# Performance work log

Hardware: AMD Instinct MI355X
Metric: run time of the kernel (lower is better)

The kernel has to match this reference:

```python
import jax, jax.numpy as jnp
import numpy as np


def setup_inputs() -> dict:
    key = jax.random.key(0)
    k1, k2 = jax.random.split(key)
    decoder_hidden = jax.random.normal(k1, (16, 1024, 1024), dtype=jnp.float32)
    encoder_outputs = jax.random.normal(k2, (16, 2048, 1024), dtype=jnp.float32)
    return {"decoder_hidden": decoder_hidden, "encoder_outputs": encoder_outputs}


def reference(decoder_hidden, encoder_outputs):
    # scores: [B, Q, K] = decoder_hidden @ encoder_outputs^T (no scaling, per source)
    scores = jnp.einsum('bqd,bkd->bqk', decoder_hidden, encoder_outputs)
    attn = jax.nn.softmax(scores, axis=-1)
    # context: [B, Q, D]
    context = jnp.einsum('bqk,bkd->bqd', attn, encoder_outputs)
    return (context, attn)
```

## Files before the change

### kernel.cpp

```cpp
#include <hip/hip_runtime.h>


typedef __attribute__((ext_vector_type(8))) short s8v;
typedef __attribute__((ext_vector_type(4))) float f32x4;
typedef __attribute__((ext_vector_type(8))) unsigned short us8;
typedef __attribute__((ext_vector_type(4))) unsigned short us4;

__device__ inline unsigned short f2bf(float f) {
    unsigned u = __builtin_bit_cast(unsigned, f);
    u += 0x7FFFu + ((u >> 16) & 1u);
    return (unsigned short)(u >> 16);
}
__device__ inline float bf2f(unsigned short h) {
    return __builtin_bit_cast(float, (unsigned)h << 16);
}

__device__ __forceinline__ s8v lds_read128(unsigned addr) {
    s8v d;
    asm volatile("ds_read_b128 %0, %1" : "=v"(d) : "v"(addr));
    return d;
}

__global__ __launch_bounds__(256)
void split_convert(const float* __restrict__ x, unsigned short* __restrict__ hi,
                   unsigned short* __restrict__ lo, int n4)
{
    int i = blockIdx.x * 256 + threadIdx.x;
    const int stride = gridDim.x * 256;
    for (; i < n4; i += stride) {
        const float4 v = reinterpret_cast<const float4*>(x)[i];
        us4 h, l;
        h.x = f2bf(v.x); l.x = f2bf(v.x - bf2f(h.x));
        h.y = f2bf(v.y); l.y = f2bf(v.y - bf2f(h.y));
        h.z = f2bf(v.z); l.z = f2bf(v.z - bf2f(h.z));
        h.w = f2bf(v.w); l.w = f2bf(v.w - bf2f(h.w));
        reinterpret_cast<us4*>(hi)[i] = h;
        reinterpret_cast<us4*>(lo)[i] = l;
    }
}

__global__ __launch_bounds__(256)
void split_convert_enc(const float* __restrict__ enc,
                       unsigned short* __restrict__ encH,
                       unsigned short* __restrict__ encL,
                       unsigned short* __restrict__ encT)
{
    __shared__ unsigned short S[64][72];
    const int b  = blockIdx.z;
    const int kt = blockIdx.x;
    const int dt = blockIdx.y;
    const int tid = threadIdx.x;

    const int r   = tid >> 2;
    const int c16 = (tid & 3) * 16;

    const size_t inoff = (size_t)b * 2048 * 1024 + (size_t)(kt * 64 + r) * 1024 + dt * 64 + c16;
    const float4* src = reinterpret_cast<const float4*>(enc + inoff);

    us8 h0, h1, l0, l1;
    #pragma unroll
    for (int q = 0; q < 2; ++q) {
        const float4 a = src[q * 2 + 0];
        const float4 c = src[q * 2 + 1];
        us8& h = q ? h1 : h0;
        us8& l = q ? l1 : l0;
        h[0] = f2bf(a.x); l[0] = f2bf(a.x - bf2f(h[0]));
        h[1] = f2bf(a.y); l[1] = f2bf(a.y - bf2f(h[1]));
        h[2] = f2bf(a.z); l[2] = f2bf(a.z - bf2f(h[2]));
        h[3] = f2bf(a.w); l[3] = f2bf(a.w - bf2f(h[3]));
        h[4] = f2bf(c.x); l[4] = f2bf(c.x - bf2f(h[4]));
        h[5] = f2bf(c.y); l[5] = f2bf(c.y - bf2f(h[5]));
        h[6] = f2bf(c.z); l[6] = f2bf(c.z - bf2f(h[6]));
        h[7] = f2bf(c.w); l[7] = f2bf(c.w - bf2f(h[7]));
    }
    *reinterpret_cast<us8*>(&encH[inoff])     = h0;
    *reinterpret_cast<us8*>(&encH[inoff + 8]) = h1;
    *reinterpret_cast<us8*>(&encL[inoff])     = l0;
    *reinterpret_cast<us8*>(&encL[inoff + 8]) = l1;
    *reinterpret_cast<us8*>(&S[r][c16])     = h0;
    *reinterpret_cast<us8*>(&S[r][c16 + 8]) = h1;
    __syncthreads();

    const int d   = tid >> 2;
    const int k16 = (tid & 3) * 16;
    us8 w0, w1;
    #pragma unroll
    for (int j = 0; j < 8; ++j) { w0[j] = S[k16 + j][d]; w1[j] = S[k16 + 8 + j][d]; }
    const size_t outoff = (size_t)b * 1024 * 2048 + (size_t)(dt * 64 + d) * 2048 + kt * 64 + k16;
    *reinterpret_cast<us8*>(&encT[outoff])     = w0;
    *reinterpret_cast<us8*>(&encT[outoff + 8]) = w1;
}

template<int NPASS, int KPP, int NXT, int NYT>
__global__ __launch_bounds__(512, 2)
void gemm_nt_256(const unsigned short* __restrict__ A0,
                 const unsigned short* __restrict__ A1,
                 const unsigned short* __restrict__ A2,
                 const unsigned short* __restrict__ B0,
                 const unsigned short* __restrict__ B1,
                 const unsigned short* __restrict__ B2,
                 float* __restrict__ Out,
                 const int ldA, const int ldB, const int ldO,
                 const long long sA, const long long sB, const long long sO)
{
    constexpr int TPP = KPP / 32;
    constexpr int NT  = NPASS * TPP;
    extern __shared__ unsigned short smem[];

    int flat = blockIdx.x + NXT * (blockIdx.y + NYT * (int)blockIdx.z);
    const int nwg = NXT * NYT * (int)gridDim.z;
    flat = (flat & 7) * (nwg >> 3) + (flat >> 3);
    const int nt = flat % NXT;
    const int mt = (flat / NXT) % NYT;
    const int b  = flat / (NXT * NYT);

    const int tid = threadIdx.x, lane = tid & 63, wid = tid >> 6;
    const int wm = wid >> 2, wn = wid & 3;

    const size_t arow = (size_t)b * sA + (size_t)(mt * 256) * ldA;
    const size_t brow = (size_t)b * sB + (size_t)(nt * 256) * ldB;
    const unsigned short* Ap0 = A0 + arow;
    const unsigned short* Ap1 = A1 + arow;
    const unsigned short* Ap2 = A2 + arow;
    const unsigned short* Bp0 = B0 + brow;
    const unsigned short* Bp1 = B1 + brow;
    const unsigned short* Bp2 = B2 + brow;

    const int ci0 = tid, ci1 = 512 + tid;
    const int r0 = ci0 >> 2, r1 = ci1 >> 2;
    const int cs0 = ((ci0 & 3) ^ ((r0 >> 1) & 3)) * 8;
    const int cs1 = ((ci1 & 3) ^ ((r1 >> 1) & 3)) * 8;
    const int aoff0 = r0 * ldA + cs0, aoff1 = r1 * ldA + cs1;
    const int boff0 = r0 * ldB + cs0, boff1 = r1 * ldB + cs1;
    const int wd0 = wid * 512;
    const int wd1 = 4096 + wid * 512;

    auto stageA = [&](int t) {
        const int p  = t / TPP;
        const int k0 = (t % TPP) * 32;
        const unsigned short* As = (p == 0) ? Ap0 : (p == 1 ? Ap1 : Ap2);
        unsigned short* d = smem + (t & 3) * 16384;
        __builtin_amdgcn_global_load_lds(
            (const __attribute__((address_space(1))) void*)(As + k0 + aoff0),
            (__attribute__((address_space(3))) void*)(d + wd0), 16, 0, 0);
        __builtin_amdgcn_global_load_lds(
            (const __attribute__((address_space(1))) void*)(As + k0 + aoff1),
            (__attribute__((address_space(3))) void*)(d + wd1), 16, 0, 0);
    };
    auto stageB = [&](int t) {
        const int p  = t / TPP;
        const int k0 = (t % TPP) * 32;
        const unsigned short* Bs = (p == 0) ? Bp0 : (p == 1 ? Bp1 : Bp2);
        unsigned short* d = smem + (t & 3) * 16384 + 8192;
        __builtin_amdgcn_global_load_lds(
            (const __attribute__((address_space(1))) void*)(Bs + k0 + boff0),
            (__attribute__((address_space(3))) void*)(d + wd0), 16, 0, 0);
        __builtin_amdgcn_global_load_lds(
            (const __attribute__((address_space(1))) void*)(Bs + k0 + boff1),
            (__attribute__((address_space(3))) void*)(d + wd1), 16, 0, 0);
    };

    const int fr = lane & 15;
    const int kc = lane >> 4;
    unsigned offA[8], offB[4];
    #pragma unroll
    for (int m = 0; m < 8; ++m) {
        const int R = wm * 128 + m * 16 + fr;
        offA[m] = (unsigned)(R * 64) + ((unsigned)(kc ^ ((R >> 1) & 3)) << 4);
    }
    #pragma unroll
    for (int n = 0; n < 4; ++n) {
        const int R = wn * 64 + n * 16 + fr;
        offB[n] = 16384u + (unsigned)(R * 64) + ((unsigned)(kc ^ ((R >> 1) & 3)) << 4);
    }

    const unsigned lds0 =
        (unsigned)(uintptr_t)(__attribute__((address_space(3))) unsigned short*)smem;

    f32x4 acc[8][4];
    #pragma unroll
    for (int m = 0; m < 8; ++m)
        #pragma unroll
        for (int n = 0; n < 4; ++n) acc[m][n] = (f32x4){0.f, 0.f, 0.f, 0.f};

    stageA(0); stageB(0); stageA(1); stageB(1); stageA(2); stageB(2);
    asm volatile("s_waitcnt vmcnt(4)" ::: "memory");
    __builtin_amdgcn_s_barrier();

    s8v fA[8], fB[4], gA[8], gB[4];
    #pragma unroll
    for (int n = 0; n < 4; ++n) fB[n] = lds_read128(lds0 + offB[n]);
    #pragma unroll
    for (int m = 0; m < 8; ++m) fA[m] = lds_read128(lds0 + offA[m]);

    auto tile_body = [&](const int t, s8v (&ca)[8], s8v (&cb)[4],
                         s8v (&na)[8], s8v (&nb)[4], const bool reads) {
        const unsigned nbase = lds0 + (unsigned)((t + 1) & 3) * 32768u;
        __builtin_amdgcn_s_setprio(1);

        if (reads) {
            nb[0] = lds_read128(nbase + offB[0]);
            nb[1] = lds_read128(nbase + offB[1]);
            nb[2] = lds_read128(nbase + offB[2]);
            nb[3] = lds_read128(nbase + offB[3]);
            na[0] = lds_read128(nbase + offA[0]);
            na[1] = lds_read128(nbase + offA[1]);
            asm volatile("s_waitcnt lgkmcnt(12)" ::: "memory");
        } else {
            asm volatile("s_waitcnt lgkmcnt(6)" ::: "memory");
        }
        __builtin_amdgcn_sched_barrier(0);
        #pragma unroll
        for (int m = 0; m < 2; ++m)
            #pragma unroll
            for (int n = 0; n < 4; ++n)
                acc[m][n] = __builtin_amdgcn_mfma_f32_16x16x32_bf16(ca[m], cb[n], acc[m][n], 0, 0, 0);

        if (reads) {
            na[2] = lds_read128(nbase + offA[2]);
            na[3] = lds_read128(nbase + offA[3]);
            asm volatile("s_waitcnt lgkmcnt(12)" ::: "memory");
        } else {
            asm volatile("s_waitcnt lgkmcnt(4)" ::: "memory");
        }
        __builtin_amdgcn_sched_barrier(0);
        #pragma unroll
        for (int m = 2; m < 4; ++m)
            #pragma unroll
            for (int n = 0; n < 4; ++n)
                acc[m][n] = __builtin_amdgcn_mfma_f32_16x16x32_bf16(ca[m], cb[n], acc[m][n], 0, 0, 0);

        if (t + 3 < NT) { stageA(t + 3); stageB(t + 3); }

        if (reads) {
            na[4] = lds_read128(nbase + offA[4]);
            na[5] = lds_read128(nbase + offA[5]);
            asm volatile("s_waitcnt lgkmcnt(12)" ::: "memory");
        } else {
            asm volatile("s_waitcnt lgkmcnt(2)" ::: "memory");
        }
        __builtin_amdgcn_sched_barrier(0);
        #pragma unroll
        for (int m = 4; m < 6; ++m)
            #pragma unroll
            for (int n = 0; n < 4; ++n)
                acc[m][n] = __builtin_amdgcn_mfma_f32_16x16x32_bf16(ca[m], cb[n], acc[m][n], 0, 0, 0);

        if (reads) {
            na[6] = lds_read128(nbase + offA[6]);
            na[7] = lds_read128(nbase + offA[7]);
            asm volatile("s_waitcnt lgkmcnt(12)" ::: "memory");
        } else {
            asm volatile("s_waitcnt lgkmcnt(0)" ::: "memory");
        }
        __builtin_amdgcn_sched_barrier(0);
        #pragma unroll
        for (int m = 6; m < 8; ++m)
            #pragma unroll
            for (int n = 0; n < 4; ++n)
                acc[m][n] = __builtin_amdgcn_mfma_f32_16x16x32_bf16(ca[m], cb[n], acc[m][n], 0, 0, 0);
        __builtin_amdgcn_s_setprio(0);

        if (t + 3 < NT)      asm volatile("s_waitcnt vmcnt(4)" ::: "memory");
        else if (t + 2 < NT) asm volatile("s_waitcnt vmcnt(0)" ::: "memory");
        __builtin_amdgcn_s_barrier();
    };

    for (int tt = 0; tt < NT - 2; tt += 2) {
        tile_body(tt,     fA, fB, gA, gB, true);
        tile_body(tt + 1, gA, gB, fA, fB, true);
    }
    tile_body(NT - 2, fA, fB, gA, gB, true);
    tile_body(NT - 1, gA, gB, fA, fB, false);

    float* Ob = Out + (size_t)b * sO + (size_t)(mt * 256 + wm * 128) * ldO + nt * 256 + wn * 64;
    const int cr = (lane >> 4) << 2;
    const int cc = lane & 15;
    #pragma unroll
    for (int m = 0; m < 8; ++m)
        #pragma unroll
        for (int n = 0; n < 4; ++n)
            #pragma unroll
            for (int r = 0; r < 4; ++r)
                Ob[(size_t)(m * 16 + cr + r) * ldO + n * 16 + cc] = acc[m][n][r];
}

__global__ __launch_bounds__(256)
void softmax_rows_bf(float* __restrict__ P, unsigned short* __restrict__ Pb)
{
    float* p = P + (size_t)blockIdx.x * 2048;
    unsigned short* pb = Pb + (size_t)blockIdx.x * 2048;
    const int tid = threadIdx.x;

    float4 v0 = *reinterpret_cast<const float4*>(&p[tid * 4]);
    float4 v1 = *reinterpret_cast<const float4*>(&p[1024 + tid * 4]);

    float m = fmaxf(fmaxf(fmaxf(v0.x, v0.y), fmaxf(v0.z, v0.w)),
                    fmaxf(fmaxf(v1.x, v1.y), fmaxf(v1.z, v1.w)));
    #pragma unroll
    for (int off = 32; off; off >>= 1) m = fmaxf(m, __shfl_xor(m, off));

    __shared__ float red[8];
    const int wid = tid >> 6;
    if ((tid & 63) == 0) red[wid] = m;
    __syncthreads();
    m = fmaxf(fmaxf(red[0], red[1]), fmaxf(red[2], red[3]));

    v0.x = __expf(v0.x - m); v0.y = __expf(v0.y - m);
    v0.z = __expf(v0.z - m); v0.w = __expf(v0.w - m);
    v1.x = __expf(v1.x - m); v1.y = __expf(v1.y - m);
    v1.z = __expf(v1.z - m); v1.w = __expf(v1.w - m);

    float s = ((v0.x + v0.y) + (v0.z + v0.w)) + ((v1.x + v1.y) + (v1.z + v1.w));
    #pragma unroll
    for (int off = 32; off; off >>= 1) s += __shfl_xor(s, off);
    if ((tid & 63) == 0) red[4 + wid] = s;
    __syncthreads();
    const float inv = 1.0f / ((red[4] + red[5]) + (red[6] + red[7]));

    v0.x *= inv; v0.y *= inv; v0.z *= inv; v0.w *= inv;
    v1.x *= inv; v1.y *= inv; v1.z *= inv; v1.w *= inv;
    *reinterpret_cast<float4*>(&p[tid * 4]) = v0;
    *reinterpret_cast<float4*>(&p[1024 + tid * 4]) = v1;

    us4 h0, h1;
    h0.x = f2bf(v0.x); h0.y = f2bf(v0.y); h0.z = f2bf(v0.z); h0.w = f2bf(v0.w);
    h1.x = f2bf(v1.x); h1.y = f2bf(v1.y); h1.z = f2bf(v1.z); h1.w = f2bf(v1.w);
    *reinterpret_cast<us4*>(&pb[tid * 4]) = h0;
    *reinterpret_cast<us4*>(&pb[1024 + tid * 4]) = h1;
}

#define BM 128
#define BN 128
#define BK 32
#define LDT 132

template <bool TRANSB>
__global__ __launch_bounds__(256, 2)
void gemm_tile(const float* __restrict__ X, const float* __restrict__ Y,
               float* __restrict__ Out,
               int ldX, int ldY, int ldO, int KD,
               long long strideX, long long strideY, long long strideO)
{
    __shared__ float As[BK][LDT];
    __shared__ float Bs[BK][LDT];
    const int b  = blockIdx.z;
    const int mt = blockIdx.y;
    const int nt = blockIdx.x;
    const float* Xb = X + (size_t)b * strideX + (size_t)mt * BM * ldX;
    const float* Yb = TRANSB ? (Y + (size_t)b * strideY + (size_t)nt * BN * ldY)
                             : (Y + (size_t)b * strideY + (size_t)nt * BN);
    float* Ob = Out + (size_t)b * strideO + (size_t)mt * BM * ldO + (size_t)nt * BN;
    const int tid = threadIdx.x;
    const int tx = tid & 15;
    const int ty = tid >> 4;
    const int sr = tid >> 3;
    const int sc = (tid & 7) << 2;
    const int br = tid >> 5;
    const int bc = (tid & 31) << 2;
    float acc[8][8];
    #pragma unroll
    for (int i = 0; i < 8; ++i)
        #pragma unroll
        for (int j = 0; j < 8; ++j) acc[i][j] = 0.f;
    for (int k0 = 0; k0 < KD; k0 += BK) {
        #pragma unroll
        for (int p = 0; p < 4; ++p) {
            const float4 v = *reinterpret_cast<const float4*>(
                &Xb[(size_t)(sr + 32 * p) * ldX + k0 + sc]);
            As[sc + 0][sr + 32 * p] = v.x;
            As[sc + 1][sr + 32 * p] = v.y;
            As[sc + 2][sr + 32 * p] = v.z;
            As[sc + 3][sr + 32 * p] = v.w;
        }
        if (TRANSB) {
            #pragma unroll
            for (int p = 0; p < 4; ++p) {
                const float4 v = *reinterpret_cast<const float4*>(
                    &Yb[(size_t)(sr + 32 * p) * ldY + k0 + sc]);
                Bs[sc + 0][sr + 32 * p] = v.x;
                Bs[sc + 1][sr + 32 * p] = v.y;
                Bs[sc + 2][sr + 32 * p] = v.z;
                Bs[sc + 3][sr + 32 * p] = v.w;
            }
        } else {
            #pragma unroll
            for (int p = 0; p < 4; ++p) {
                const float4 v = *reinterpret_cast<const float4*>(
                    &Yb[(size_t)(k0 + br + 8 * p) * ldY + bc]);
                *reinterpret_cast<float4*>(&Bs[br + 8 * p][bc]) = v;
            }
        }
        __syncthreads();
        #pragma unroll 8
        for (int kk = 0; kk < BK; ++kk) {
            const float4 a0 = *reinterpret_cast<const float4*>(&As[kk][ty * 4]);
            const float4 a1 = *reinterpret_cast<const float4*>(&As[kk][64 + ty * 4]);
            const float4 b0 = *reinterpret_cast<const float4*>(&Bs[kk][tx * 4]);
            const float4 b1 = *reinterpret_cast<const float4*>(&Bs[kk][64 + tx * 4]);
            const float av[8] = {a0.x, a0.y, a0.z, a0.w, a1.x, a1.y, a1.z, a1.w};
            const float bv[8] = {b0.x, b0.y, b0.z, b0.w, b1.x, b1.y, b1.z, b1.w};
            #pragma unroll
            for (int i = 0; i < 8; ++i)
                #pragma unroll
                for (int j = 0; j < 8; ++j)
                    acc[i][j] = fmaf(av[i], bv[j], acc[i][j]);
        }
        __syncthreads();
    }
    #pragma unroll
    for (int i = 0; i < 8; ++i) {
        const int r = (i < 4) ? (ty * 4 + i) : (64 + ty * 4 + (i - 4));
        const float4 w0 = make_float4(acc[i][0], acc[i][1], acc[i][2], acc[i][3]);
        const float4 w1 = make_float4(acc[i][4], acc[i][5], acc[i][6], acc[i][7]);
        *reinterpret_cast<float4*>(&Ob[(size_t)r * ldO + tx * 4])      = w0;
        *reinterpret_cast<float4*>(&Ob[(size_t)r * ldO + 64 + tx * 4]) = w1;
    }
}

__global__ __launch_bounds__(256)
void softmax_rows(float* __restrict__ P)
{
    float* p = P + (size_t)blockIdx.x * 2048;
    const int tid = threadIdx.x;
    float4 v0 = *reinterpret_cast<const float4*>(&p[tid * 4]);
    float4 v1 = *reinterpret_cast<const float4*>(&p[1024 + tid * 4]);
    float m = fmaxf(fmaxf(fmaxf(v0.x, v0.y), fmaxf(v0.z, v0.w)),
                    fmaxf(fmaxf(v1.x, v1.y), fmaxf(v1.z, v1.w)));
    #pragma unroll
    for (int off = 32; off; off >>= 1) m = fmaxf(m, __shfl_xor(m, off));
    __shared__ float red[8];
    const int wid = tid >> 6;
    if ((tid & 63) == 0) red[wid] = m;
    __syncthreads();
    m = fmaxf(fmaxf(red[0], red[1]), fmaxf(red[2], red[3]));
    v0.x = __expf(v0.x - m); v0.y = __expf(v0.y - m);
    v0.z = __expf(v0.z - m); v0.w = __expf(v0.w - m);
    v1.x = __expf(v1.x - m); v1.y = __expf(v1.y - m);
    v1.z = __expf(v1.z - m); v1.w = __expf(v1.w - m);
    float s = ((v0.x + v0.y) + (v0.z + v0.w)) + ((v1.x + v1.y) + (v1.z + v1.w));
    #pragma unroll
    for (int off = 32; off; off >>= 1) s += __shfl_xor(s, off);
    if ((tid & 63) == 0) red[4 + wid] = s;
    __syncthreads();
    const float inv = 1.0f / ((red[4] + red[5]) + (red[6] + red[7]));
    v0.x *= inv; v0.y *= inv; v0.z *= inv; v0.w *= inv;
    v1.x *= inv; v1.y *= inv; v1.z *= inv; v1.w *= inv;
    *reinterpret_cast<float4*>(&p[tid * 4]) = v0;
    *reinterpret_cast<float4*>(&p[1024 + tid * 4]) = v1;
}

extern "C" void kernel_launch(void* const* d_in, const int* in_sizes, int n_in,
                              void* d_out, int out_size, void* d_ws, size_t ws_size,
                              hipStream_t stream)
{
    const float* dec = (const float*)d_in[0];
    const float* enc = (const float*)d_in[1];
    float* ctx  = (float*)d_out;
    float* attn = ctx + (size_t)16 * 1024 * 1024;

    const long long DECN = 16LL * 1024 * 1024;
    const long long ENCN = 16LL * 2048 * 1024;
    const size_t NEED = (size_t)(2 * DECN + 4 * ENCN) * 2;

    if (ws_size >= NEED) {
        unsigned short* decH  = (unsigned short*)d_ws;
        unsigned short* decL  = decH + DECN;
        unsigned short* encH  = decL + DECN;
        unsigned short* encL  = encH + ENCN;
        unsigned short* encT  = encL + ENCN;
        unsigned short* attnB = encT + ENCN;

        hipFuncSetAttribute((const void*)&gemm_nt_256<3, 1024, 8, 4>,
                            hipFuncAttributeMaxDynamicSharedMemorySize, 131072);
        hipFuncSetAttribute((const void*)&gemm_nt_256<1, 2048, 4, 4>,
                            hipFuncAttributeMaxDynamicSharedMemorySize, 131072);

        split_convert<<<2048, 256, 0, stream>>>(dec, decH, decL, (int)(DECN / 4));
        split_convert_enc<<<dim3(32, 16, 16), 256, 0, stream>>>(enc, encH, encL, encT);

        gemm_nt_256<3, 1024, 8, 4><<<dim3(8, 4, 16), 512, 131072, stream>>>(
            decH, decH, decL, encH, encL, encH, attn,
            1024, 1024, 2048,
            1024LL * 1024, 2048LL * 1024, 1024LL * 2048);

        softmax_rows_bf<<<16 * 1024, 256, 0, stream>>>(attn, attnB);

        gemm_nt_256<1, 2048, 4, 4><<<dim3(4, 4, 16), 512, 131072, stream>>>(
            attnB, attnB, attnB, encT, encT, encT, ctx,
            2048, 2048, 1024,
            1024LL * 2048, 1024LL * 2048, 1024LL * 1024);
    } else {
        gemm_tile<true><<<dim3(2048 / BN, 1024 / BM, 16), 256, 0, stream>>>(
            dec, enc, attn, 1024, 1024, 2048, 1024,
            1024LL * 1024, 2048LL * 1024, 1024LL * 2048);
        softmax_rows<<<dim3(16 * 1024), 256, 0, stream>>>(attn);
        gemm_tile<false><<<dim3(1024 / BN, 1024 / BM, 16), 256, 0, stream>>>(
            attn, enc, ctx, 2048, 1024, 1024, 2048,
            1024LL * 2048, 2048LL * 1024, 1024LL * 1024);
    }
}
```

Baseline: 422.9 us.

## Split GEMM waves into two groups with staggered LDS-read and MFMA phases

Replaces the finely interleaved per-tile schedule, where LDS fragment reads were spread between MFMA groups, with a warp-specialized ping-pong. Waves 0-3 issue all next-tile LDS reads before their MFMA block. Waves 4-7 run their MFMA block first and read afterwards, so one group's LDS traffic overlaps the other group's matrix math. The global prefetch for tile t+3 is moved to the start of each tile. The risk is losing intra-wave latency hiding: waves now wait on lgkmcnt(0) right before their MFMAs, which can stall them if the other group does not keep the matrix units busy.

Measured after the change: 419.7 us. Within noise of the previous version (-0.7%).

```diff
diff --git a/kernel.cpp b/kernel.cpp
--- a/kernel.cpp
+++ b/kernel.cpp
@@ -193,85 +193,64 @@
     #pragma unroll
     for (int m = 0; m < 8; ++m) fA[m] = lds_read128(lds0 + offA[m]);
 
-    auto tile_body = [&](const int t, s8v (&ca)[8], s8v (&cb)[4],
-                         s8v (&na)[8], s8v (&nb)[4], const bool reads) {
+    auto issue_reads = [&](const int t, s8v (&na)[8], s8v (&nb)[4]) {
         const unsigned nbase = lds0 + (unsigned)((t + 1) & 3) * 32768u;
+        #pragma unroll
+        for (int n = 0; n < 4; ++n) nb[n] = lds_read128(nbase + offB[n]);
+        #pragma unroll
+        for (int m = 0; m < 8; ++m) na[m] = lds_read128(nbase + offA[m]);
+    };
+    auto do_mfma = [&](s8v (&ca)[8], s8v (&cb)[4]) {
         __builtin_amdgcn_s_setprio(1);
-
-        if (reads) {
-            nb[0] = lds_read128(nbase + offB[0]);
-            nb[1] = lds_read128(nbase + offB[1]);
-            nb[2] = lds_read128(nbase + offB[2]);
-            nb[3] = lds_read128(nbase + offB[3]);
-            na[0] = lds_read128(nbase + offA[0]);
-            na[1] = lds_read128(nbase + offA[1]);
-            asm volatile("s_waitcnt lgkmcnt(12)" ::: "memory");
-        } else {
-            asm volatile("s_waitcnt lgkmcnt(6)" ::: "memory");
-        }
-        __builtin_amdgcn_sched_barrier(0);
-        #pragma unroll
-        for (int m = 0; m < 2; ++m)
-            #pragma unroll
-            for (int n = 0; n < 4; ++n)
-                acc[m][n] = __builtin_amdgcn_mfma_f32_16x16x32_bf16(ca[m], cb[n], acc[m][n], 0, 0, 0);
-
-        if (reads) {
-            na[2] = lds_read128(nbase + offA[2]);
-            na[3] = lds_read128(nbase + offA[3]);
-            asm volatile("s_waitcnt lgkmcnt(12)" ::: "memory");
-        } else {
-            asm volatile("s_waitcnt lgkmcnt(4)" ::: "memory");
-        }
-        __builtin_amdgcn_sched_barrier(0);
-        #pragma unroll
-        for (int m = 2; m < 4; ++m)
-            #pragma unroll
-            for (int n = 0; n < 4; ++n)
-                acc[m][n] = __builtin_amdgcn_mfma_f32_16x16x32_bf16(ca[m], cb[n], acc[m][n], 0, 0, 0);
-
-        if (t + 3 < NT) { stageA(t + 3); stageB(t + 3); }
-
-        if (reads) {
-            na[4] = lds_read128(nbase + offA[4]);
-            na[5] = lds_read128(nbase + offA[5]);
-            asm volatile("s_waitcnt lgkmcnt(12)" ::: "memory");
-        } else {
-            asm volatile("s_waitcnt lgkmcnt(2)" ::: "memory");
-        }
-        __builtin_amdgcn_sched_barrier(0);
-        #pragma unroll
-        for (int m = 4; m < 6; ++m)
-            #pragma unroll
-            for (int n = 0; n < 4; ++n)
-                acc[m][n] = __builtin_amdgcn_mfma_f32_16x16x32_bf16(ca[m], cb[n], acc[m][n], 0, 0, 0);
-
-        if (reads) {
-            na[6] = lds_read128(nbase + offA[6]);
-            na[7] = lds_read128(nbase + offA[7]);
-            asm volatile("s_waitcnt lgkmcnt(12)" ::: "memory");
-        } else {
-            asm volatile("s_waitcnt lgkmcnt(0)" ::: "memory");
-        }
-        __builtin_amdgcn_sched_barrier(0);
-        #pragma unroll
-        for (int m = 6; m < 8; ++m)
+        #pragma unroll
+        for (int m = 0; m < 8; ++m)
             #pragma unroll
             for (int n = 0; n < 4; ++n)
                 acc[m][n] = __builtin_amdgcn_mfma_f32_16x16x32_bf16(ca[m], cb[n], acc[m][n], 0, 0, 0);
         __builtin_amdgcn_s_setprio(0);
-
+    };
+    auto tail_sync = [&](const int t) {
         if (t + 3 < NT)      asm volatile("s_waitcnt vmcnt(4)" ::: "memory");
         else if (t + 2 < NT) asm volatile("s_waitcnt vmcnt(0)" ::: "memory");
         __builtin_amdgcn_s_barrier();
     };
 
-    for (int tt = 0; tt < NT - 2; tt += 2) {
-        tile_body(tt,     fA, fB, gA, gB, true);
-        tile_body(tt + 1, gA, gB, fA, fB, true);
-    }
-    tile_body(NT - 2, fA, fB, gA, gB, true);
-    tile_body(NT - 1, gA, gB, fA, fB, false);
+    auto bodyA = [&](const int t, s8v (&ca)[8], s8v (&cb)[4],
+                     s8v (&na)[8], s8v (&nb)[4], const bool reads) {
+        if (t + 3 < NT) { stageA(t + 3); stageB(t + 3); }
+        if (reads) {
+            issue_reads(t, na, nb);
+            asm volatile("s_waitcnt lgkmcnt(12)" ::: "memory");
+        } else {
+            asm volatile("s_waitcnt lgkmcnt(0)" ::: "memory");
+        }
+        __builtin_amdgcn_sched_barrier(0);
+        do_mfma(ca, cb);
+        __builtin_amdgcn_sched_barrier(0);
+        tail_sync(t);
+    };
+    auto bodyB = [&](const int t, s8v (&ca)[8], s8v (&cb)[4],
+                     s8v (&na)[8], s8v (&nb)[4], const bool reads) {
+        if (t + 3 < NT) { stageA(t + 3); stageB(t + 3); }
+        asm volatile("s_waitcnt lgkmcnt(0)" ::: "memory");
+        __builtin_amdgcn_sched_barrier(0);
+        do_mfma(ca, cb);
+        __builtin_amdgcn_sched_barrier(0);
+        if (reads) issue_reads(t, na, nb);
+        tail_sync(t);
+    };
+
+    if (wid < 4) {
+        for (int tt = 0; tt < NT; tt += 2) {
+            bodyA(tt,     fA, fB, gA, gB, true);
+            bodyA(tt + 1, gA, gB, fA, fB, tt + 2 < NT);
+        }
+    } else {
+        for (int tt = 0; tt < NT; tt += 2) {
+            bodyB(tt,     fA, fB, gA, gB, true);
+            bodyB(tt + 1, gA, gB, fA, fB, tt + 2 < NT);
+        }
+    }
 
     float* Ob = Out + (size_t)b * sO + (size_t)(mt * 256 + wm * 128) * ldO + nt * 256 + wn * 64;
     const int cr = (lane >> 4) << 2;
```
